# Kernel optimization log

Hardware: AMD Instinct MI355X
Metric: run time of the kernel (lower is better)

## Reference

```python
import jax, jax.numpy as jnp
import numpy as np

HEADS, HEAD_DIM = 4, 16
EDGE_DIM = 128
INNER = HEADS * HEAD_DIM  # 64


def _ln(x, g, b, eps=1e-5):
    m = jnp.mean(x, axis=-1, keepdims=True)
    v = jnp.var(x, axis=-1, keepdims=True)
    return (x - m) * jax.lax.rsqrt(v + eps) * g + b


def _gated_attention(x, ln_g, ln_b, w_qkv, w_gate, b_gate, w_fin, b_fin):
    # x: (b, n, d)
    b, n, _ = x.shape
    normed = _ln(x, ln_g, ln_b)
    qkv = normed @ w_qkv.T                      # (b, n, 3*INNER)
    q, k, v = jnp.split(qkv, 3, axis=-1)
    to_heads = lambda t: t.reshape(b, n, HEADS, HEAD_DIM).transpose(0, 2, 1, 3)
    q, k, v = to_heads(q), to_heads(k), to_heads(v)
    gate = jax.nn.sigmoid(to_heads(x @ w_gate.T + b_gate))  # (b, h, n, d)
    attn = jnp.einsum('bhid,bhjd->bhij', q, k) * HEAD_DIM ** -0.5
    p = jax.nn.softmax(attn, axis=-1)
    # Faithful to source: 'bhij,bhid->bhjd' contracts over i (= P^T V)
    out = jnp.einsum('bhij,bhid->bhjd', p, v) * gate
    out = out.transpose(0, 2, 1, 3).reshape(b, n, INNER)
    return x + out @ w_fin.T + b_fin


def setup_inputs() -> dict:
    key = jax.random.key(0)
    ks = jax.random.split(key, 16)
    L, D = 384, EDGE_DIM
    s = 0.02
    inp = {
        'edge_features': jax.random.normal(ks[0], (L, L, D), jnp.float32),
        # row attention params
        'r_ln_g': jnp.ones((D,), jnp.float32),
        'r_ln_b': jnp.zeros((D,), jnp.float32),
        'r_qkv_w': jax.random.normal(ks[1], (3 * INNER, D), jnp.float32) * s,
        'r_gate_w': jax.random.normal(ks[2], (INNER, D), jnp.float32) * s,
        'r_gate_b': jnp.ones((INNER,), jnp.float32),
        'r_fin_w': jax.random.normal(ks[3], (D, INNER), jnp.float32) * s,
        'r_fin_b': jnp.zeros((D,), jnp.float32),
        # column attention params
        'c_ln_g': jnp.ones((D,), jnp.float32),
        'c_ln_b': jnp.zeros((D,), jnp.float32),
        'c_qkv_w': jax.random.normal(ks[4], (3 * INNER, D), jnp.float32) * s,
        'c_gate_w': jax.random.normal(ks[5], (INNER, D), jnp.float32) * s,
        'c_gate_b': jnp.ones((INNER,), jnp.float32),
        'c_fin_w': jax.random.normal(ks[6], (D, INNER), jnp.float32) * s,
        'c_fin_b': jnp.zeros((D,), jnp.float32),
        # feed-forward params
        'ff_w1': jax.random.normal(ks[7], (2 * D, D), jnp.float32) * s,
        'ff_b1': jnp.zeros((2 * D,), jnp.float32),
        'ff_w2': jax.random.normal(ks[8], (D, 2 * D), jnp.float32) * s,
        'ff_b2': jnp.zeros((D,), jnp.float32),
    }
    return inp


def reference(edge_features, r_ln_g, r_ln_b, r_qkv_w, r_gate_w, r_gate_b, r_fin_w, r_fin_b,
              c_ln_g, c_ln_b, c_qkv_w, c_gate_w, c_gate_b, c_fin_w, c_fin_b,
              ff_w1, ff_b1, ff_w2, ff_b2):
    x = _gated_attention(edge_features, r_ln_g, r_ln_b, r_qkv_w, r_gate_w, r_gate_b, r_fin_w, r_fin_b)
    x = x.transpose(1, 0, 2)
    x = _gated_attention(x, c_ln_g, c_ln_b, c_qkv_w, c_gate_w, c_gate_b, c_fin_w, c_fin_b)
    x = x.transpose(1, 0, 2)
    h = jax.nn.silu(x) @ ff_w1.T + ff_b1
    h = jax.nn.silu(h) @ ff_w2.T + ff_b2
    return x + h
```

## Files before the change

kernel.cpp:

```cpp
#include <hip/hip_runtime.h>

#define LSEQ 384
#define DIM 128
#define NHEADS 4
#define HDIM 16

typedef __attribute__((ext_vector_type(8))) short bf16x8;
typedef __attribute__((ext_vector_type(4))) short bf16x4;
typedef __attribute__((ext_vector_type(4))) float f32x4;

#define MFMA32(A,B,C) __builtin_amdgcn_mfma_f32_16x16x32_bf16(A,B,C,0,0,0)

#if __has_builtin(__builtin_amdgcn_mfma_f32_16x16x16bf16_1k)
#define HAVE_MFMA16 1
#else
#define HAVE_MFMA16 0
#endif

__device__ __forceinline__ float bf2f_lo(unsigned int u) { return __uint_as_float(u << 16); }
__device__ __forceinline__ float bf2f_hi(unsigned int u) { return __uint_as_float(u & 0xFFFF0000u); }
__device__ __forceinline__ float bf2f_s(unsigned short s) { return __uint_as_float(((unsigned int)s) << 16); }
__device__ __forceinline__ unsigned short f2bf(float f) {
    unsigned int u = __float_as_uint(f);
    u += 0x7FFFu + ((u >> 16) & 1u);
    return (unsigned short)(u >> 16);
}
__device__ __forceinline__ unsigned int pkbf(float a, float b) {
    unsigned int r;
    asm("v_cvt_pk_bf16_f32 %0, %1, %2" : "=v"(r) : "v"(a), "v"(b));
    return r;
}
__device__ __forceinline__ float ex2(float x) {
#if __has_builtin(__builtin_amdgcn_exp2f)
    return __builtin_amdgcn_exp2f(x);
#else
    return exp2f(x);
#endif
}
__device__ __forceinline__ float frcp(float x) {
#if __has_builtin(__builtin_amdgcn_rcpf)
    return __builtin_amdgcn_rcpf(x);
#else
    return 1.f / x;
#endif
}
__device__ __forceinline__ float fsigm(float x) {
    return frcp(1.f + ex2(-1.44269504088896341f * x));
}
__device__ __forceinline__ float fsilu(float x) { return x * fsigm(x); }
__device__ __forceinline__ bf16x8 ldw8(const unsigned short* p) {
    union { uint4 x; bf16x8 v; } c;
    c.x = *(const uint4*)p;
    return c.v;
}


__global__ __launch_bounds__(256) void wconv_kernel(
    const float* __restrict__ r_qkv_w, const float* __restrict__ r_gate_w,
    const float* __restrict__ c_qkv_w, const float* __restrict__ c_gate_w,
    const float* __restrict__ ff_w1, const float* __restrict__ ff_w2,
    const float* __restrict__ r_fin_w, const float* __restrict__ c_fin_w,
    unsigned short* __restrict__ wout)
{
    int idx = blockIdx.x * 256 + threadIdx.x;
    const float SQ = 0.36067376022224085f;
    float2 a;
    if (idx < 32768) {
        int half = idx >> 14;
        int e = (idx & 16383) * 2;
        int row = e >> 7, col = e & 127;
        const float* qkv = half ? c_qkv_w : r_qkv_w;
        const float* gw  = half ? c_gate_w : r_gate_w;
        const float* src = (row < 192) ? (qkv + (long)row * 128 + col)
                                       : (gw + (long)(row - 192) * 128 + col);
        a = *(const float2*)src;
        if (row < 64) { a.x *= SQ; a.y *= SQ; }
    } else if (idx < 49152) {
        a = *(const float2*)(ff_w1 + (long)(idx - 32768) * 2);
    } else if (idx < 65536) {
        a = *(const float2*)(ff_w2 + (long)(idx - 49152) * 2);
    } else if (idx < 69632) {
        a = *(const float2*)(r_fin_w + (long)(idx - 65536) * 2);
    } else {
        a = *(const float2*)(c_fin_w + (long)(idx - 69632) * 2);
    }
    ((unsigned int*)wout)[idx] = pkbf(a.x, a.y);
}

#define XSTR 138
__global__ __launch_bounds__(256, 3) void qkvg_kernel(
    const float* __restrict__ x, long sb, long sn,
    const float* __restrict__ ln_g, const float* __restrict__ ln_b,
    const unsigned short* __restrict__ wqg,
    const float* __restrict__ b_gate,
    unsigned short* __restrict__ qws, unsigned short* __restrict__ kws,
    unsigned short* __restrict__ vws, unsigned short* __restrict__ gws)
{
    const int b   = blockIdx.x;
    const int q4  = blockIdx.y;
    const int tid = threadIdx.x, wave = tid >> 6, lane = tid & 63;
    const int jl  = lane & 15, g = lane >> 4;

    __shared__ __align__(16) unsigned short xn[96 * XSTR];
    __shared__ __align__(16) unsigned short xr[96 * XSTR];

    bf16x8 wfrag[4][4];
#pragma unroll
    for (int t = 0; t < 4; ++t) {
        int c = (wave * 4 + t) * 16 + jl;
        const unsigned short* wr = wqg + (long)c * 128;
#pragma unroll
        for (int ks = 0; ks < 4; ++ks) wfrag[t][ks] = ldw8(wr + ks * 32 + g * 8);
    }
    float4 gb4[4];
    if (wave == 3) {
#pragma unroll
        for (int t = 0; t < 4; ++t) gb4[t] = *(const float4*)(b_gate + t * 16 + g * 4);
    }

    const float* xbase = x + (long)b * sb + (long)(q4 * 96) * sn;
    const float4 lgA = *(const float4*)(ln_g + jl * 8);
    const float4 lgB = *(const float4*)(ln_g + jl * 8 + 4);
    const float4 lbA = *(const float4*)(ln_b + jl * 8);
    const float4 lbB = *(const float4*)(ln_b + jl * 8 + 4);
#pragma unroll
    for (int i = 0; i < 6; ++i) {
        int tk = wave * 24 + i * 4 + g;
        const float* xp = xbase + (long)tk * sn + jl * 8;
        float4 a0 = *(const float4*)xp;
        float4 a1 = *(const float4*)(xp + 4);
        float s  = ((a0.x + a0.y) + (a0.z + a0.w)) + ((a1.x + a1.y) + (a1.z + a1.w));
        float sq = a0.x * a0.x;
        sq = fmaf(a0.y, a0.y, sq); sq = fmaf(a0.z, a0.z, sq); sq = fmaf(a0.w, a0.w, sq);
        sq = fmaf(a1.x, a1.x, sq); sq = fmaf(a1.y, a1.y, sq);
        sq = fmaf(a1.z, a1.z, sq); sq = fmaf(a1.w, a1.w, sq);
        s  += __shfl_xor(s, 1, 64);  sq += __shfl_xor(sq, 1, 64);
        s  += __shfl_xor(s, 2, 64);  sq += __shfl_xor(sq, 2, 64);
        s  += __shfl_xor(s, 4, 64);  sq += __shfl_xor(sq, 4, 64);
        s  += __shfl_xor(s, 8, 64);  sq += __shfl_xor(sq, 8, 64);
        float mean = s * (1.f / 128.f);
        float var  = sq * (1.f / 128.f) - mean * mean;
        float inv  = rsqrtf(var + 1e-5f);
        float n0 = (a0.x - mean) * inv * lgA.x + lbA.x;
        float n1 = (a0.y - mean) * inv * lgA.y + lbA.y;
        float n2 = (a0.z - mean) * inv * lgA.z + lbA.z;
        float n3 = (a0.w - mean) * inv * lgA.w + lbA.w;
        float n4 = (a1.x - mean) * inv * lgB.x + lbB.x;
        float n5 = (a1.y - mean) * inv * lgB.y + lbB.y;
        float n6 = (a1.z - mean) * inv * lgB.z + lbB.z;
        float n7 = (a1.w - mean) * inv * lgB.w + lbB.w;
        unsigned int* dn = (unsigned int*)(xn + tk * XSTR) + jl * 4;
        dn[0] = pkbf(n0, n1); dn[1] = pkbf(n2, n3);
        dn[2] = pkbf(n4, n5); dn[3] = pkbf(n6, n7);
        unsigned int* dr = (unsigned int*)(xr + tk * XSTR) + jl * 4;
        dr[0] = pkbf(a0.x, a0.y); dr[1] = pkbf(a0.z, a0.w);
        dr[2] = pkbf(a1.x, a1.y); dr[3] = pkbf(a1.z, a1.w);
    }
    __syncthreads();

    const unsigned int* a32 = (const unsigned int*)((wave == 3) ? xr : xn);
    for (int mt = 0; mt < 6; ++mt) {
        bf16x8 af[4];
#pragma unroll
        for (int ks = 0; ks < 4; ++ks) {
            int adw = (mt * 16 + jl) * (XSTR / 2) + ks * 16 + g * 4;
            union { unsigned int u[4]; bf16x8 v; } cv;
            cv.u[0] = a32[adw]; cv.u[1] = a32[adw + 1];
            cv.u[2] = a32[adw + 2]; cv.u[3] = a32[adw + 3];
            af[ks] = cv.v;
        }
#pragma unroll
        for (int t = 0; t < 4; ++t) {
            int nt = wave * 4 + t;
            f32x4 acc = {0.f, 0.f, 0.f, 0.f};
#pragma unroll
            for (int ks = 0; ks < 4; ++ks) acc = MFMA32(wfrag[t][ks], af[ks], acc);
            int mat = nt >> 2, hh = nt & 3;
            int token = q4 * 96 + mt * 16 + jl;
            long base = (((long)b * NHEADS + hh) * LSEQ + token) * HDIM + g * 4;
            if (mat == 3) {
                float4 gb = gb4[t];
                float v0 = fsigm(acc[0] + gb.x), v1 = fsigm(acc[1] + gb.y);
                float v2 = fsigm(acc[2] + gb.z), v3 = fsigm(acc[3] + gb.w);
                uint2 pk = { pkbf(v0, v1), pkbf(v2, v3) };
                *(uint2*)(gws + base) = pk;
            } else {
                unsigned short* outp = (mat == 0) ? qws : (mat == 1) ? kws : vws;
                uint2 pk = { pkbf(acc[0], acc[1]), pkbf(acc[2], acc[3]) };
                *(uint2*)(outp + base) = pk;
            }
        }
    }
}

#if HAVE_MFMA16
typedef bf16x4 sfrag_t;
#define SMFMA(A,B,C) __builtin_amdgcn_mfma_f32_16x16x16bf16_1k(A,B,C,0,0,0)
__device__ __forceinline__ sfrag_t ldfragG(const unsigned short* base, int row, int g) {
    union { uint2 x; bf16x4 v; } c;
    c.x = *(const uint2*)(base + row * 16 + g * 4);
    return c.v;
}
#else
typedef bf16x8 sfrag_t;
#define SMFMA(A,B,C) MFMA32(A,B,C)
__device__ __forceinline__ sfrag_t ldfragG(const unsigned short* base, int row, int g) {
    union { uint4 x; bf16x8 v; } c;
    if (g < 2) c.x = *(const uint4*)(base + row * 16 + g * 8);
    else { c.x.x = 0; c.x.y = 0; c.x.z = 0; c.x.w = 0; }
    return c.v;
}
#endif

__global__ __launch_bounds__(256, 4) void attn_core_kernel(
    const unsigned short* __restrict__ qws, const unsigned short* __restrict__ kws,
    const unsigned short* __restrict__ vws, const unsigned short* __restrict__ gws,
    unsigned short* __restrict__ attn_out)
{
    const int b = blockIdx.x, h = blockIdx.y;
    const int tid = threadIdx.x, wave = tid >> 6, lane = tid & 63;
    const int jl  = lane & 15, g = lane >> 4;

    __shared__ float linv[LSEQ];

    const long goff = ((long)b * NHEADS + h) * (LSEQ * HDIM);
    const unsigned short* Q = qws + goff;
    const unsigned short* K = kws + goff;
    const unsigned short* V = vws + goff;

    uint2 gq6[6];
#pragma unroll
    for (int t = 0; t < 6; ++t)
        gq6[t] = *(const uint2*)(gws + goff + (long)((wave * 6 + t) * 16 + jl) * 16 + g * 4);

    sfrag_t Qo[6], Ko[6];
#pragma unroll
    for (int t = 0; t < 6; ++t) {
        Qo[t] = ldfragG(Q, (wave * 6 + t) * 16 + jl, g);
        Ko[t] = ldfragG(K, (wave * 6 + t) * 16 + jl, g);
    }

    const f32x4 fz = {0.f, 0.f, 0.f, 0.f};

    float lsum[6] = {0.f, 0.f, 0.f, 0.f, 0.f, 0.f};
    {
        sfrag_t kc0 = ldfragG(K, jl, g), kc1 = ldfragG(K, 16 + jl, g);
        for (int u = 0; u < 12; ++u) {
            sfrag_t c0 = kc0, c1 = kc1;
            if (u < 11) {
                kc0 = ldfragG(K, 32 * (u + 1) + jl, g);
                kc1 = ldfragG(K, 32 * (u + 1) + 16 + jl, g);
            }
#pragma unroll
            for (int t = 0; t < 6; ++t) {
                f32x4 s0 = SMFMA(c0, Qo[t], fz);
                f32x4 s1 = SMFMA(c1, Qo[t], fz);
                lsum[t] += ((ex2(s0[0]) + ex2(s0[1])) + (ex2(s0[2]) + ex2(s0[3])))
                         + ((ex2(s1[0]) + ex2(s1[1])) + (ex2(s1[2]) + ex2(s1[3])));
            }
        }
    }
#pragma unroll
    for (int t = 0; t < 6; ++t) {
        float l = lsum[t];
        l += __shfl_xor(l, 16, 64);
        l += __shfl_xor(l, 32, 64);
        if (lane < 16) linv[(wave * 6 + t) * 16 + jl] = 1.f / l;
    }

    sfrag_t qc0 = ldfragG(Q, jl, g), qc1 = ldfragG(Q, 16 + jl, g);
    unsigned short vv[8];
#pragma unroll
    for (int p = 0; p < 4; ++p) {
        int t0 = (p < 2) ? (g * 4 + 2 * p) : (16 + g * 4 + 2 * (p - 2));
        vv[2 * p]     = V[t0 * 16 + jl];
        vv[2 * p + 1] = V[(t0 + 1) * 16 + jl];
    }
    __syncthreads();

    f32x4 o[6];
#pragma unroll
    for (int t = 0; t < 6; ++t) o[t] = fz;

    for (int u = 0; u < 12; ++u) {
        union { unsigned int w[4]; bf16x8 v; } vbu;
#pragma unroll
        for (int p = 0; p < 4; ++p) {
            int t0 = 32 * u + ((p < 2) ? (g * 4 + 2 * p) : (16 + g * 4 + 2 * (p - 2)));
            vbu.w[p] = pkbf(bf2f_s(vv[2 * p]) * linv[t0],
                            bf2f_s(vv[2 * p + 1]) * linv[t0 + 1]);
        }
        bf16x8 VB = vbu.v;
        sfrag_t c0 = qc0, c1 = qc1;
        if (u < 11) {
            qc0 = ldfragG(Q, 32 * (u + 1) + jl, g);
            qc1 = ldfragG(Q, 32 * (u + 1) + 16 + jl, g);
#pragma unroll
            for (int p = 0; p < 4; ++p) {
                int t0 = 32 * (u + 1) + ((p < 2) ? (g * 4 + 2 * p) : (16 + g * 4 + 2 * (p - 2)));
                vv[2 * p]     = V[t0 * 16 + jl];
                vv[2 * p + 1] = V[(t0 + 1) * 16 + jl];
            }
        }
#pragma unroll
        for (int t = 0; t < 6; ++t) {
            f32x4 s0 = SMFMA(c0, Ko[t], fz);
            f32x4 s1 = SMFMA(c1, Ko[t], fz);
            union { unsigned int w[4]; bf16x8 v; } pf;
            pf.w[0] = pkbf(ex2(s0[0]), ex2(s0[1]));
            pf.w[1] = pkbf(ex2(s0[2]), ex2(s0[3]));
            pf.w[2] = pkbf(ex2(s1[0]), ex2(s1[1]));
            pf.w[3] = pkbf(ex2(s1[2]), ex2(s1[3]));
            o[t] = MFMA32(VB, pf.v, o[t]);
        }
    }

#pragma unroll
    for (int t = 0; t < 6; ++t) {
        int jrow = (wave * 6 + t) * 16 + jl;
        uint2 gpk = gq6[t];
        float r0 = o[t][0] * bf2f_lo(gpk.x);
        float r1 = o[t][1] * bf2f_hi(gpk.x);
        float r2 = o[t][2] * bf2f_lo(gpk.y);
        float r3 = o[t][3] * bf2f_hi(gpk.y);
        uint2 pk = { pkbf(r0, r1), pkbf(r2, r3) };
        *(uint2*)(attn_out + ((long)b * LSEQ + jrow) * 64 + h * HDIM + g * 4) = pk;
    }
}

__global__ __launch_bounds__(256, 4) void fin_kernel(
    const unsigned short* __restrict__ A,
    const unsigned short* __restrict__ Wb, const float* __restrict__ Bv,
    const float* __restrict__ R, long rs0, long rs1,
    float* __restrict__ out, long os0, long os1)
{
    const int tid = threadIdx.x, wave = tid >> 6, lane = tid & 63;
    const int jl = lane & 15, g = lane >> 4;

    bf16x8 wfrag[2][2];
    float4 bias4[2];
#pragma unroll
    for (int t = 0; t < 2; ++t) {
        int c = (wave * 2 + t) * 16 + jl;
        const unsigned short* wr = Wb + (long)c * 64;
        bias4[t] = *(const float4*)(Bv + (wave * 2 + t) * 16 + g * 4);
        wfrag[t][0] = ldw8(wr + g * 8);
        wfrag[t][1] = ldw8(wr + 32 + g * 8);
    }

    const long t0 = (long)blockIdx.x * 96;
    const int i0 = blockIdx.x >> 2;
    const int j0b = (blockIdx.x & 3) * 96;

    for (int mt = 0; mt < 6; ++mt) {
        const unsigned short* ap = A + (t0 + mt * 16 + jl) * 64;
        bf16x8 af0 = ldw8(ap + g * 8);
        bf16x8 af1 = ldw8(ap + 32 + g * 8);
#pragma unroll
        for (int t = 0; t < 2; ++t) {
            f32x4 acc = {0.f, 0.f, 0.f, 0.f};
            acc = MFMA32(wfrag[t][0], af0, acc);
            acc = MFMA32(wfrag[t][1], af1, acc);
            int tj = j0b + mt * 16 + jl;
            long cbase = (wave * 2 + t) * 16 + g * 4;
            float4 rq = *(const float4*)(R + (long)i0 * rs0 + (long)tj * rs1 + cbase);
            float4 bq = bias4[t];
            float4 vv;
            vv.x = acc[0] + bq.x + rq.x;
            vv.y = acc[1] + bq.y + rq.y;
            vv.z = acc[2] + bq.z + rq.z;
            vv.w = acc[3] + bq.w + rq.w;
            *(float4*)(out + (long)i0 * os0 + (long)tj * os1 + cbase) = vv;
        }
    }
}

__global__ __launch_bounds__(256, 3) void ff_fused_kernel(
    const float* __restrict__ Y,
    const unsigned short* __restrict__ W1b, const float* __restrict__ B1,
    const unsigned short* __restrict__ W2b, const float* __restrict__ B2,
    float* __restrict__ out)
{
    const int tid = threadIdx.x, wave = tid >> 6, lane = tid & 63;
    const int jl = lane & 15, g = lane >> 4;

    __shared__ __align__(16) unsigned int hs[96 * 132];

    bf16x8 w1f[4][4];
    float4 b1q[4];
#pragma unroll
    for (int t = 0; t < 4; ++t) {
        int c = wave * 64 + t * 16 + jl;
        const unsigned short* wr = W1b + (long)c * 128;
        b1q[t] = *(const float4*)(B1 + wave * 64 + t * 16 + g * 4);
#pragma unroll
        for (int ks = 0; ks < 4; ++ks) w1f[t][ks] = ldw8(wr + ks * 32 + g * 8);
    }

    const long t0 = (long)blockIdx.x * 96;

    for (int mt = 0; mt < 6; ++mt) {
        const float* ap = Y + (t0 + mt * 16 + jl) * 128;
        bf16x8 af[4];
#pragma unroll
        for (int ks = 0; ks < 4; ++ks) {
            float4 a0 = *(const float4*)(ap + ks * 32 + g * 8);
            float4 a1 = *(const float4*)(ap + ks * 32 + g * 8 + 4);
            union { unsigned int u[4]; bf16x8 v; } cv;
            cv.u[0] = pkbf(fsilu(a0.x), fsilu(a0.y));
            cv.u[1] = pkbf(fsilu(a0.z), fsilu(a0.w));
            cv.u[2] = pkbf(fsilu(a1.x), fsilu(a1.y));
            cv.u[3] = pkbf(fsilu(a1.z), fsilu(a1.w));
            af[ks] = cv.v;
        }
#pragma unroll
        for (int t = 0; t < 4; ++t) {
            f32x4 acc = {0.f, 0.f, 0.f, 0.f};
#pragma unroll
            for (int ks = 0; ks < 4; ++ks) acc = MFMA32(w1f[t][ks], af[ks], acc);
            float4 bq = b1q[t];
            float h0 = fsilu(acc[0] + bq.x), h1 = fsilu(acc[1] + bq.y);
            float h2 = fsilu(acc[2] + bq.z), h3 = fsilu(acc[3] + bq.w);
            uint2 pk = { pkbf(h0, h1), pkbf(h2, h3) };
            *(uint2*)(hs + (mt * 16 + jl) * 132 + wave * 32 + t * 8 + g * 2) = pk;
        }
    }

    bf16x8 w2f[2][8];
    float4 b2q[2];
#pragma unroll
    for (int t = 0; t < 2; ++t) {
        int co = wave * 32 + t * 16 + jl;
        const unsigned short* wr = W2b + (long)co * 256;
        b2q[t] = *(const float4*)(B2 + wave * 32 + t * 16 + g * 4);
#pragma unroll
        for (int ks = 0; ks < 8; ++ks) w2f[t][ks] = ldw8(wr + ks * 32 + g * 8);
    }
    __syncthreads();

    const int i0 = blockIdx.x >> 2;
    const int j0b = (blockIdx.x & 3) * 96;

    for (int mt = 0; mt < 6; ++mt) {
        bf16x8 af[8];
#pragma unroll
        for (int ks = 0; ks < 8; ++ks) {
            int adw = (mt * 16 + jl) * 132 + ks * 16 + g * 4;
            uint4 x = *(const uint4*)(hs + adw);
            union { unsigned int u[4]; bf16x8 v; } cv;
            cv.u[0] = x.x; cv.u[1] = x.y; cv.u[2] = x.z; cv.u[3] = x.w;
            af[ks] = cv.v;
        }
#pragma unroll
        for (int t = 0; t < 2; ++t) {
            f32x4 acc = {0.f, 0.f, 0.f, 0.f};
#pragma unroll
            for (int ks = 0; ks < 8; ++ks) acc = MFMA32(w2f[t][ks], af[ks], acc);
            int tj = j0b + mt * 16 + jl;
            long cbase = wave * 32 + t * 16 + g * 4;
            long addr = (long)i0 * 49152 + (long)tj * 128 + cbase;
            float4 rq = *(const float4*)(Y + addr);
            float4 bq = b2q[t];
            float4 vv;
            vv.x = acc[0] + bq.x + rq.x;
            vv.y = acc[1] + bq.y + rq.y;
            vv.z = acc[2] + bq.z + rq.z;
            vv.w = acc[3] + bq.w + rq.w;
            *(float4*)(out + addr) = vv;
        }
    }
}

extern "C" void kernel_launch(void* const* d_in, const int* in_sizes, int n_in,
                              void* d_out, int out_size, void* d_ws, size_t ws_size,
                              hipStream_t stream)
{
    const float* edge     = (const float*)d_in[0];
    const float* r_ln_g   = (const float*)d_in[1];
    const float* r_ln_b   = (const float*)d_in[2];
    const float* r_qkv_w  = (const float*)d_in[3];
    const float* r_gate_w = (const float*)d_in[4];
    const float* r_gate_b = (const float*)d_in[5];
    const float* r_fin_w  = (const float*)d_in[6];
    const float* r_fin_b  = (const float*)d_in[7];
    const float* c_ln_g   = (const float*)d_in[8];
    const float* c_ln_b   = (const float*)d_in[9];
    const float* c_qkv_w  = (const float*)d_in[10];
    const float* c_gate_w = (const float*)d_in[11];
    const float* c_gate_b = (const float*)d_in[12];
    const float* c_fin_w  = (const float*)d_in[13];
    const float* c_fin_b  = (const float*)d_in[14];
    const float* ff_w1    = (const float*)d_in[15];
    const float* ff_b1    = (const float*)d_in[16];
    const float* ff_w2    = (const float*)d_in[17];
    const float* ff_b2    = (const float*)d_in[18];

    char* ws = (char*)d_ws;
    unsigned short* qb = (unsigned short*)ws;
    unsigned short* kb = qb + 9437184;
    unsigned short* vb = qb + 2 * 9437184;
    unsigned short* gb = qb + 3 * 9437184;
    unsigned short* attnb = (unsigned short*)(ws + 75497472);
    unsigned short* wcv   = (unsigned short*)(ws + 75497472 + 18874368);
    float* y    = (float*)(ws + 75497472 + 37748736);

    const unsigned short* wqg_r = wcv;
    const unsigned short* wqg_c = wcv + 32768;
    const unsigned short* w1b   = wcv + 65536;
    const unsigned short* w2b   = wcv + 98304;
    const unsigned short* wfin_r = wcv + 131072;
    const unsigned short* wfin_c = wcv + 139264;

    const long LD = 49152;

    wconv_kernel<<<288, 256, 0, stream>>>(
        r_qkv_w, r_gate_w, c_qkv_w, c_gate_w, ff_w1, ff_w2, r_fin_w, c_fin_w, wcv);

    qkvg_kernel<<<dim3(LSEQ, 4), 256, 0, stream>>>(
        edge, LD, 128, r_ln_g, r_ln_b, wqg_r, r_gate_b, qb, kb, vb, gb);
    attn_core_kernel<<<dim3(LSEQ, NHEADS), 256, 0, stream>>>(qb, kb, vb, gb, attnb);
    fin_kernel<<<1536, 256, 0, stream>>>(
        attnb, wfin_r, r_fin_b, edge, LD, 128, y, LD, 128);

    qkvg_kernel<<<dim3(LSEQ, 4), 256, 0, stream>>>(
        y, 128, LD, c_ln_g, c_ln_b, wqg_c, c_gate_b, qb, kb, vb, gb);
    attn_core_kernel<<<dim3(LSEQ, NHEADS), 256, 0, stream>>>(qb, kb, vb, gb, attnb);
    fin_kernel<<<1536, 256, 0, stream>>>(
        attnb, wfin_c, c_fin_b, y, 128, LD, y, 128, LD);

    ff_fused_kernel<<<1536, 256, 0, stream>>>(
        y, w1b, ff_b1, w2b, ff_b2, (float*)d_out);
}
```

Measured before the change: 459.4 us.

## Prefetch FFN inputs and residuals one tile ahead; raise occupancy hints

The FFN kernel now loads the next 16-row tile of Y into registers while the current tile is being processed, in both the first GEMM and the residual-add phase. This is meant to hide global-load latency behind the MFMA work. The attention-core and final-projection kernels also raise their launch-bounds occupancy hint from 4 to 6 blocks, which caps registers per thread and may cause spills. The prefetch buffers add register pressure to the FFN kernel.

```diff
diff --git a/kernel.cpp b/kernel.cpp
--- a/kernel.cpp
+++ b/kernel.cpp
@@ -212,7 +212,7 @@
 }
 #endif
 
-__global__ __launch_bounds__(256, 4) void attn_core_kernel(
+__global__ __launch_bounds__(256, 6) void attn_core_kernel(
     const unsigned short* __restrict__ qws, const unsigned short* __restrict__ kws,
     const unsigned short* __restrict__ vws, const unsigned short* __restrict__ gws,
     unsigned short* __restrict__ attn_out)
@@ -328,7 +328,7 @@
     }
 }
 
-__global__ __launch_bounds__(256, 4) void fin_kernel(
+__global__ __launch_bounds__(256, 6) void fin_kernel(
     const unsigned short* __restrict__ A,
     const unsigned short* __restrict__ Wb, const float* __restrict__ Bv,
     const float* __restrict__ R, long rs0, long rs1,
@@ -399,13 +399,27 @@
 
     const long t0 = (long)blockIdx.x * 96;
 
+    float4 pa[8];
+    {
+        const float* ap = Y + (t0 + jl) * 128;
+#pragma unroll
+        for (int q = 0; q < 8; ++q)
+            pa[q] = *(const float4*)(ap + (q >> 1) * 32 + g * 8 + (q & 1) * 4);
+    }
     for (int mt = 0; mt < 6; ++mt) {
-        const float* ap = Y + (t0 + mt * 16 + jl) * 128;
+        float4 cur[8];
+#pragma unroll
+        for (int q = 0; q < 8; ++q) cur[q] = pa[q];
+        if (mt < 5) {
+            const float* apn = Y + (t0 + (mt + 1) * 16 + jl) * 128;
+#pragma unroll
+            for (int q = 0; q < 8; ++q)
+                pa[q] = *(const float4*)(apn + (q >> 1) * 32 + g * 8 + (q & 1) * 4);
+        }
         bf16x8 af[4];
 #pragma unroll
         for (int ks = 0; ks < 4; ++ks) {
-            float4 a0 = *(const float4*)(ap + ks * 32 + g * 8);
-            float4 a1 = *(const float4*)(ap + ks * 32 + g * 8 + 4);
+            float4 a0 = cur[2 * ks], a1 = cur[2 * ks + 1];
             union { unsigned int u[4]; bf16x8 v; } cv;
             cv.u[0] = pkbf(fsilu(a0.x), fsilu(a0.y));
             cv.u[1] = pkbf(fsilu(a0.z), fsilu(a0.w));
@@ -440,8 +454,21 @@
 
     const int i0 = blockIdx.x >> 2;
     const int j0b = (blockIdx.x & 3) * 96;
-
+    const long cb0 = wave * 32 + g * 4;
+
+    float4 pr0, pr1;
+    {
+        long ad = (long)i0 * 49152 + (long)(j0b + jl) * 128 + cb0;
+        pr0 = *(const float4*)(Y + ad);
+        pr1 = *(const float4*)(Y + ad + 16);
+    }
     for (int mt = 0; mt < 6; ++mt) {
+        float4 cr0 = pr0, cr1 = pr1;
+        if (mt < 5) {
+            long adn = (long)i0 * 49152 + (long)(j0b + (mt + 1) * 16 + jl) * 128 + cb0;
+            pr0 = *(const float4*)(Y + adn);
+            pr1 = *(const float4*)(Y + adn + 16);
+        }
         bf16x8 af[8];
 #pragma unroll
         for (int ks = 0; ks < 8; ++ks) {
@@ -457,9 +484,8 @@
 #pragma unroll
             for (int ks = 0; ks < 8; ++ks) acc = MFMA32(w2f[t][ks], af[ks], acc);
             int tj = j0b + mt * 16 + jl;
-            long cbase = wave * 32 + t * 16 + g * 4;
-            long addr = (long)i0 * 49152 + (long)tj * 128 + cbase;
-            float4 rq = *(const float4*)(Y + addr);
+            long addr = (long)i0 * 49152 + (long)tj * 128 + cb0 + t * 16;
+            float4 rq = t ? cr1 : cr0;
             float4 bq = b2q[t];
             float4 vv;
             vv.x = acc[0] + bq.x + rq.x;
```

Measured after the change: 472.5 us. +2.9%, slower.

## Fuse column-attention output projection into feed-forward kernel

Applied to the files above, without the earlier changes.

Merges the column fin projection (plus residual) into the feed-forward kernel, so the intermediate y is held in registers instead of being written to and re-read from global memory. The FF hidden layer is now processed in two halves of 128 channels, accumulating the second GEMM across halves. This uses smaller shared buffers and loads weights per half. In exchange it adds register pressure (yreg and acc2 arrays), extra barriers, and a strided gather of attention output rows.

```diff
diff --git a/kernel.cpp b/kernel.cpp
--- a/kernel.cpp
+++ b/kernel.cpp
@@ -375,8 +375,10 @@
     }
 }
 
-__global__ __launch_bounds__(256, 3) void ff_fused_kernel(
-    const float* __restrict__ Y,
+__global__ __launch_bounds__(256, 3) void finff_kernel(
+    const unsigned short* __restrict__ A,
+    const unsigned short* __restrict__ Wfin, const float* __restrict__ Bfin,
+    const float* __restrict__ R,
     const unsigned short* __restrict__ W1b, const float* __restrict__ B1,
     const unsigned short* __restrict__ W2b, const float* __restrict__ B2,
     float* __restrict__ out)
@@ -384,88 +386,137 @@
     const int tid = threadIdx.x, wave = tid >> 6, lane = tid & 63;
     const int jl = lane & 15, g = lane >> 4;
 
-    __shared__ __align__(16) unsigned int hs[96 * 132];
-
-    bf16x8 w1f[4][4];
-    float4 b1q[4];
-#pragma unroll
-    for (int t = 0; t < 4; ++t) {
-        int c = wave * 64 + t * 16 + jl;
-        const unsigned short* wr = W1b + (long)c * 128;
-        b1q[t] = *(const float4*)(B1 + wave * 64 + t * 16 + g * 4);
-#pragma unroll
-        for (int ks = 0; ks < 4; ++ks) w1f[t][ks] = ldw8(wr + ks * 32 + g * 8);
-    }
-
-    const long t0 = (long)blockIdx.x * 96;
-
+    __shared__ __align__(16) unsigned int xs[96 * 66];
+    __shared__ __align__(16) unsigned int hsh[96 * 66];
+
+    const int i0  = blockIdx.x >> 2;
+    const int j0b = (blockIdx.x & 3) * 96;
+
+    f32x4 yreg[6][2];
+    {
+        bf16x8 wf[2][2];
+        float4 bf4[2];
+#pragma unroll
+        for (int t = 0; t < 2; ++t) {
+            int c = (wave * 2 + t) * 16 + jl;
+            const unsigned short* wr = Wfin + (long)c * 64;
+            wf[t][0] = ldw8(wr + g * 8);
+            wf[t][1] = ldw8(wr + 32 + g * 8);
+            bf4[t] = *(const float4*)(Bfin + (wave * 2 + t) * 16 + g * 4);
+        }
+#pragma unroll
+        for (int mt = 0; mt < 6; ++mt) {
+            int col = j0b + mt * 16 + jl;
+            const unsigned short* ap = A + ((long)col * 384 + i0) * 64;
+            bf16x8 a0 = ldw8(ap + g * 8);
+            bf16x8 a1 = ldw8(ap + 32 + g * 8);
+#pragma unroll
+            for (int t = 0; t < 2; ++t) {
+                f32x4 acc = {0.f, 0.f, 0.f, 0.f};
+                acc = MFMA32(wf[t][0], a0, acc);
+                acc = MFMA32(wf[t][1], a1, acc);
+                long cbase = (wave * 2 + t) * 16 + g * 4;
+                float4 rq = *(const float4*)(R + (long)i0 * 49152 + (long)col * 128 + cbase);
+                float4 bq = bf4[t];
+                f32x4 yv;
+                yv[0] = acc[0] + bq.x + rq.x;
+                yv[1] = acc[1] + bq.y + rq.y;
+                yv[2] = acc[2] + bq.z + rq.z;
+                yv[3] = acc[3] + bq.w + rq.w;
+                yreg[mt][t] = yv;
+                unsigned int* dx = xs + (mt * 16 + jl) * 66 + wave * 16 + t * 8 + g * 2;
+                dx[0] = pkbf(fsilu(yv[0]), fsilu(yv[1]));
+                dx[1] = pkbf(fsilu(yv[2]), fsilu(yv[3]));
+            }
+        }
+    }
+    __syncthreads();
+
+    f32x4 acc2[6][2];
+#pragma unroll
     for (int mt = 0; mt < 6; ++mt) {
-        const float* ap = Y + (t0 + mt * 16 + jl) * 128;
-        bf16x8 af[4];
-#pragma unroll
-        for (int ks = 0; ks < 4; ++ks) {
-            float4 a0 = *(const float4*)(ap + ks * 32 + g * 8);
-            float4 a1 = *(const float4*)(ap + ks * 32 + g * 8 + 4);
-            union { unsigned int u[4]; bf16x8 v; } cv;
-            cv.u[0] = pkbf(fsilu(a0.x), fsilu(a0.y));
-            cv.u[1] = pkbf(fsilu(a0.z), fsilu(a0.w));
-            cv.u[2] = pkbf(fsilu(a1.x), fsilu(a1.y));
-            cv.u[3] = pkbf(fsilu(a1.z), fsilu(a1.w));
-            af[ks] = cv.v;
-        }
-#pragma unroll
-        for (int t = 0; t < 4; ++t) {
-            f32x4 acc = {0.f, 0.f, 0.f, 0.f};
-#pragma unroll
-            for (int ks = 0; ks < 4; ++ks) acc = MFMA32(w1f[t][ks], af[ks], acc);
-            float4 bq = b1q[t];
-            float h0 = fsilu(acc[0] + bq.x), h1 = fsilu(acc[1] + bq.y);
-            float h2 = fsilu(acc[2] + bq.z), h3 = fsilu(acc[3] + bq.w);
-            uint2 pk = { pkbf(h0, h1), pkbf(h2, h3) };
-            *(uint2*)(hs + (mt * 16 + jl) * 132 + wave * 32 + t * 8 + g * 2) = pk;
-        }
-    }
-
-    bf16x8 w2f[2][8];
+        acc2[mt][0] = (f32x4){0.f, 0.f, 0.f, 0.f};
+        acc2[mt][1] = (f32x4){0.f, 0.f, 0.f, 0.f};
+    }
+
+#pragma unroll
+    for (int half = 0; half < 2; ++half) {
+        bf16x8 w1f[2][4];
+        float4 b1q[2];
+#pragma unroll
+        for (int t = 0; t < 2; ++t) {
+            int hc = half * 128 + wave * 32 + t * 16 + jl;
+            const unsigned short* wr = W1b + (long)hc * 128;
+#pragma unroll
+            for (int ks = 0; ks < 4; ++ks) w1f[t][ks] = ldw8(wr + ks * 32 + g * 8);
+            b1q[t] = *(const float4*)(B1 + half * 128 + wave * 32 + t * 16 + g * 4);
+        }
+        if (half == 1) __syncthreads();
+#pragma unroll
+        for (int mt = 0; mt < 6; ++mt) {
+            bf16x8 af[4];
+#pragma unroll
+            for (int ks = 0; ks < 4; ++ks) {
+                union { uint4 x; bf16x8 v; } cv;
+                cv.x = *(const uint4*)(xs + (mt * 16 + jl) * 66 + ks * 16 + g * 4);
+                af[ks] = cv.v;
+            }
+#pragma unroll
+            for (int t = 0; t < 2; ++t) {
+                f32x4 acc = {0.f, 0.f, 0.f, 0.f};
+#pragma unroll
+                for (int ks = 0; ks < 4; ++ks) acc = MFMA32(w1f[t][ks], af[ks], acc);
+                float4 bq = b1q[t];
+                unsigned int* dh = hsh + (mt * 16 + jl) * 66 + wave * 16 + t * 8 + g * 2;
+                dh[0] = pkbf(fsilu(acc[0] + bq.x), fsilu(acc[1] + bq.y));
+                dh[1] = pkbf(fsilu(acc[2] + bq.z), fsilu(acc[3] + bq.w));
+            }
+        }
+        __syncthreads();
+        bf16x8 w2f[2][4];
+#pragma unroll
+        for (int t = 0; t < 2; ++t) {
+            int co = wave * 32 + t * 16 + jl;
+            const unsigned short* wr = W2b + (long)co * 256 + half * 128;
+#pragma unroll
+            for (int ks = 0; ks < 4; ++ks) w2f[t][ks] = ldw8(wr + ks * 32 + g * 8);
+        }
+#pragma unroll
+        for (int mt = 0; mt < 6; ++mt) {
+            bf16x8 af[4];
+#pragma unroll
+            for (int ks = 0; ks < 4; ++ks) {
+                union { uint4 x; bf16x8 v; } cv;
+                cv.x = *(const uint4*)(hsh + (mt * 16 + jl) * 66 + ks * 16 + g * 4);
+                af[ks] = cv.v;
+            }
+#pragma unroll
+            for (int t = 0; t < 2; ++t) {
+#pragma unroll
+                for (int ks = 0; ks < 4; ++ks)
+                    acc2[mt][t] = MFMA32(w2f[t][ks], af[ks], acc2[mt][t]);
+            }
+        }
+    }
+
     float4 b2q[2];
 #pragma unroll
-    for (int t = 0; t < 2; ++t) {
-        int co = wave * 32 + t * 16 + jl;
-        const unsigned short* wr = W2b + (long)co * 256;
+    for (int t = 0; t < 2; ++t)
         b2q[t] = *(const float4*)(B2 + wave * 32 + t * 16 + g * 4);
 #pragma unroll
-        for (int ks = 0; ks < 8; ++ks) w2f[t][ks] = ldw8(wr + ks * 32 + g * 8);
-    }
-    __syncthreads();
-
-    const int i0 = blockIdx.x >> 2;
-    const int j0b = (blockIdx.x & 3) * 96;
-
     for (int mt = 0; mt < 6; ++mt) {
-        bf16x8 af[8];
-#pragma unroll
-        for (int ks = 0; ks < 8; ++ks) {
-            int adw = (mt * 16 + jl) * 132 + ks * 16 + g * 4;
-            uint4 x = *(const uint4*)(hs + adw);
-            union { unsigned int u[4]; bf16x8 v; } cv;
-            cv.u[0] = x.x; cv.u[1] = x.y; cv.u[2] = x.z; cv.u[3] = x.w;
-            af[ks] = cv.v;
-        }
+        int col = j0b + mt * 16 + jl;
 #pragma unroll
         for (int t = 0; t < 2; ++t) {
-            f32x4 acc = {0.f, 0.f, 0.f, 0.f};
-#pragma unroll
-            for (int ks = 0; ks < 8; ++ks) acc = MFMA32(w2f[t][ks], af[ks], acc);
-            int tj = j0b + mt * 16 + jl;
-            long cbase = wave * 32 + t * 16 + g * 4;
-            long addr = (long)i0 * 49152 + (long)tj * 128 + cbase;
-            float4 rq = *(const float4*)(Y + addr);
+            long addr = (long)i0 * 49152 + (long)col * 128 + wave * 32 + t * 16 + g * 4;
             float4 bq = b2q[t];
+            f32x4 a2 = acc2[mt][t];
+            f32x4 yv = yreg[mt][t];
             float4 vv;
-            vv.x = acc[0] + bq.x + rq.x;
-            vv.y = acc[1] + bq.y + rq.y;
-            vv.z = acc[2] + bq.z + rq.z;
-            vv.w = acc[3] + bq.w + rq.w;
+            vv.x = a2[0] + bq.x + yv[0];
+            vv.y = a2[1] + bq.y + yv[1];
+            vv.z = a2[2] + bq.z + yv[2];
+            vv.w = a2[3] + bq.w + yv[3];
             *(float4*)(out + addr) = vv;
         }
     }
@@ -525,9 +576,7 @@
     qkvg_kernel<<<dim3(LSEQ, 4), 256, 0, stream>>>(
         y, 128, LD, c_ln_g, c_ln_b, wqg_c, c_gate_b, qb, kb, vb, gb);
     attn_core_kernel<<<dim3(LSEQ, NHEADS), 256, 0, stream>>>(qb, kb, vb, gb, attnb);
-    fin_kernel<<<1536, 256, 0, stream>>>(
-        attnb, wfin_c, c_fin_b, y, 128, LD, y, 128, LD);
-
-    ff_fused_kernel<<<1536, 256, 0, stream>>>(
-        y, w1b, ff_b1, w2b, ff_b2, (float*)d_out);
-}
+
+    finff_kernel<<<1536, 256, 0, stream>>>(
+        attnb, wfin_c, c_fin_b, y, w1b, ff_b1, w2b, ff_b2, (float*)d_out);
+}
```

New measurement: 441.2 us. 1.04x faster.
